# Performance work log

Measured on AMD Instinct MI355X. Metric: run time of the kernel, lower is better.

The kernel has to match this reference:

```python
import jax, jax.numpy as jnp
import numpy as np

S, B, C, H = 8192, 4, 512, 8
D = C // H
EPS = 1e-6


def setup_inputs() -> dict:
    key = jax.random.key(0)
    ks = jax.random.split(key, 11)
    scale = 1.0 / np.sqrt(C)
    return {
        "query": jax.random.normal(ks[0], (S, B, C), jnp.float32),
        "key": jax.random.normal(ks[1], (S, B, C), jnp.float32),
        "value": jax.random.normal(ks[2], (S, B, C), jnp.float32),
        "Wq": jax.random.normal(ks[3], (C, C), jnp.float32) * scale,
        "bq": jnp.zeros((C,), jnp.float32),
        "Wk": jax.random.normal(ks[4], (C, C), jnp.float32) * scale,
        "bk": jnp.zeros((C,), jnp.float32),
        "Wv": jax.random.normal(ks[5], (C, C), jnp.float32) * scale,
        "bv": jnp.zeros((C,), jnp.float32),
        "Wp": jax.random.normal(ks[6], (C, C), jnp.float32) * scale,
        "bp": jnp.zeros((C,), jnp.float32),
    }


def _elu_fm(x):
    # ELU(x) + 1 feature map
    return jax.nn.elu(x) + 1.0


def _heads(x, W, b):
    # x: [B, N, C] -> [B, H, N, D]
    y = x @ W.T + b
    Bb, N, _ = y.shape
    return y.reshape(Bb, N, H, D).transpose(0, 2, 1, 3)


def reference(query, key, value, Wq, bq, Wk, bk, Wv, bv, Wp, bp):
    # inputs [S, B, C] -> batch-first [B, S, C]
    q_in = query.transpose(1, 0, 2)
    k_in = key.transpose(1, 0, 2)
    v_in = value.transpose(1, 0, 2)

    q = _elu_fm(_heads(q_in, Wq, bq))   # [B,H,N,D]
    k = _elu_fm(_heads(k_in, Wk, bk))   # [B,H,N,D]
    v = _heads(v_in, Wv, bv)            # [B,H,N,D]

    # linear attention: O(N) kv-sum formulation
    kv = jnp.einsum('bhnd,bhnf->bhdf', k, v)       # [B,H,D,D]
    k_sum = k.sum(axis=2)                          # [B,H,D]
    qkv = jnp.einsum('bhnd,bhdf->bhnf', q, kv)     # [B,H,N,D]
    denom = jnp.einsum('bhnd,bhd->bhn', q, k_sum)  # [B,H,N]
    y = qkv / (denom[..., None] + EPS)

    # merge heads, output projection, back to [S, B, C]
    y = y.transpose(0, 2, 1, 3).reshape(q_in.shape[0], q_in.shape[1], C)
    out = y @ Wp.T + bp
    return out.transpose(1, 0, 2)
```

## Files before the change

kernel.cpp:

```cpp
#include <hip/hip_runtime.h>
#include <hip/hip_bf16.h>
#include <math.h>

#define S_LEN 8192
#define BATCH 4
#define CDIM  512
#define HEADS 8
#define DDIM  64
#define MROWS (S_LEN * BATCH)
#define EPS_F 1e-6f

typedef __attribute__((ext_vector_type(8))) short     short8_t;
typedef __attribute__((ext_vector_type(4))) float     f32x4;
typedef unsigned short ushort_t;
typedef __attribute__((ext_vector_type(8))) unsigned short ushort8_t;

static __device__ __forceinline__ ushort_t f2bf(float f) {
  __hip_bfloat16 h = __float2bfloat16(f);
  return *(ushort_t*)&h;
}

static __device__ __forceinline__ void gl2lds16(const ushort_t* g, ushort_t* l) {
  __builtin_amdgcn_global_load_lds((const __attribute__((address_space(1))) void*)g,
                                   (__attribute__((address_space(3))) void*)l,
                                   16, 0, 0);
}

__global__ __launch_bounds__(256)
void cvtW_pack(const float* __restrict__ a, const float* __restrict__ b,
               const float* __restrict__ c, const float* __restrict__ d,
               ushort_t* __restrict__ oa, ushort_t* __restrict__ ob,
               ushort_t* __restrict__ oc, ushort_t* __restrict__ od) {
  const float* src = (blockIdx.y == 0) ? a : (blockIdx.y == 1) ? b :
                     (blockIdx.y == 2) ? c : d;
  ushort_t* dst    = (blockIdx.y == 0) ? oa : (blockIdx.y == 1) ? ob :
                     (blockIdx.y == 2) ? oc : od;
  const size_t i = ((size_t)blockIdx.x * 256 + threadIdx.x) * 8;
  const int n  = (int)(i >> 9);
  const int k0 = (int)(i & 511);
  const float4 x = *(const float4*)&src[i];
  const float4 y = *(const float4*)&src[i + 4];
  ushort8_t p;
  p[0] = f2bf(x.x); p[1] = f2bf(x.y); p[2] = f2bf(x.z); p[3] = f2bf(x.w);
  p[4] = f2bf(y.x); p[5] = f2bf(y.y); p[6] = f2bf(y.z); p[7] = f2bf(y.w);
  const int kf   = k0 >> 5;
  const int lane = ((k0 >> 3) & 3) * 16 + (n & 15);
  const int nfg  = n >> 4;
  *(ushort8_t*)&dst[(((size_t)nfg * 16 + kf) * 64 + lane) * 8] = p;
}

template<int AF32, int OUTF32>
static __device__ __forceinline__
void gemm256_body(const void* __restrict__ Av, const ushort_t* __restrict__ Wpk,
                  const float* __restrict__ bias, void* __restrict__ Yv,
                  const bool act, const int m0, const int n0, ushort_t* lds) {
  const int t    = threadIdx.x;
  const int w    = t >> 6;
  const int lane = t & 63;
  const int lr   = lane & 15;
  const int lk8  = (lane >> 4) * 8;
  const int wm   = (w >> 2) * 128;
  const int wn   = (w & 3) * 64;

  const float*    Xf = (const float*)Av;
  const ushort_t* Ah = (const ushort_t*)Av;

  ushort_t* A0 = lds;
  ushort_t* A1 = lds + 16384;
  ushort_t* B0 = lds + 32768;
  ushort_t* B1 = lds + 49152;

  f32x4 ar[4][2];

  auto regloadA = [&](int kt) {
    #pragma unroll
    for (int j = 0; j < 4; ++j) {
      const int fid = w * 4 + j;
      const size_t g = (size_t)(m0 + (fid >> 1) * 16 + lr) * CDIM +
                       kt + (fid & 1) * 32 + lk8;
      ar[j][0] = __builtin_nontemporal_load((const f32x4*)&Xf[g]);
      ar[j][1] = __builtin_nontemporal_load((const f32x4*)&Xf[g + 4]);
    }
  };
  auto stageA_f32 = [&](ushort_t* Ab) {
    #pragma unroll
    for (int j = 0; j < 4; ++j) {
      const int fid = w * 4 + j;
      short8_t v;
      v[0] = (short)f2bf(ar[j][0][0]); v[1] = (short)f2bf(ar[j][0][1]);
      v[2] = (short)f2bf(ar[j][0][2]); v[3] = (short)f2bf(ar[j][0][3]);
      v[4] = (short)f2bf(ar[j][1][0]); v[5] = (short)f2bf(ar[j][1][1]);
      v[6] = (short)f2bf(ar[j][1][2]); v[7] = (short)f2bf(ar[j][1][3]);
      *(short8_t*)&lds[(Ab - lds) + (size_t)fid * 512 + lane * 8] = v;
    }
  };
  auto stageA_bf16 = [&](ushort_t* Ab, int kt) {
    #pragma unroll
    for (int j = 0; j < 4; ++j) {
      const int fid = w * 4 + j;
      const ushort_t* g = Ah + (size_t)(m0 + (fid >> 1) * 16 + lr) * CDIM +
                          kt + (fid & 1) * 32 + lk8;
      gl2lds16(g, &Ab[fid * 512]);
    }
  };
  auto stageB = [&](ushort_t* Bb, int kt) {
    #pragma unroll
    for (int j = 0; j < 4; ++j) {
      const int fid = w * 4 + j;
      const size_t idx = ((size_t)((n0 >> 4) + (fid >> 1)) * 16 +
                          (kt >> 5) + (fid & 1));
      gl2lds16(Wpk + idx * 512 + lane * 8, &Bb[fid * 512]);
    }
  };

  f32x4 acc[8][4];
  #pragma unroll
  for (int mf = 0; mf < 8; ++mf)
    #pragma unroll
    for (int nf = 0; nf < 4; ++nf)
      acc[mf][nf] = (f32x4){0.f, 0.f, 0.f, 0.f};

  auto compute = [&](const ushort_t* Ab, const ushort_t* Bb) {
    short8_t bfr[2][4];
    #pragma unroll
    for (int kf = 0; kf < 2; ++kf)
      #pragma unroll
      for (int nf = 0; nf < 4; ++nf) {
        const int fidb = ((wn >> 4) + nf) * 2 + kf;
        bfr[kf][nf] = *(const short8_t*)&Bb[fidb * 512 + lane * 8];
      }
    #pragma unroll
    for (int mf = 0; mf < 8; ++mf) {
      const int fa = ((wm >> 4) + mf) * 2;
      const short8_t a0 = *(const short8_t*)&Ab[(fa + 0) * 512 + lane * 8];
      const short8_t a1 = *(const short8_t*)&Ab[(fa + 1) * 512 + lane * 8];
      #pragma unroll
      for (int nf = 0; nf < 4; ++nf)
        acc[mf][nf] = __builtin_amdgcn_mfma_f32_16x16x32_bf16(
            a0, bfr[0][nf], acc[mf][nf], 0, 0, 0);
      #pragma unroll
      for (int nf = 0; nf < 4; ++nf)
        acc[mf][nf] = __builtin_amdgcn_mfma_f32_16x16x32_bf16(
            a1, bfr[1][nf], acc[mf][nf], 0, 0, 0);
    }
  };

  if (AF32) {
    regloadA(0);
    stageA_f32(A0);
    stageB(B0, 0);
    regloadA(64);
  } else {
    stageA_bf16(A0, 0);
    stageB(B0, 0);
  }
  __syncthreads();

  #pragma unroll
  for (int ks = 0; ks < 8; ++ks) {
    ushort_t* curA = (ks & 1) ? A1 : A0;
    ushort_t* curB = (ks & 1) ? B1 : B0;
    ushort_t* nxtA = (ks & 1) ? A0 : A1;
    ushort_t* nxtB = (ks & 1) ? B0 : B1;
    if (ks < 7) {
      if (AF32) {
        stageA_f32(nxtA);
        if (ks + 2 < 8) regloadA((ks + 2) * 64);
      } else {
        stageA_bf16(nxtA, (ks + 1) * 64);
      }
      stageB(nxtB, (ks + 1) * 64);
    }
    compute(curA, curB);
    __syncthreads();
  }

  if (OUTF32) {
    float* Yf = (float*)Yv;
    #pragma unroll
    for (int nf = 0; nf < 4; ++nf) {
      const int col = n0 + wn + nf * 16 + lr;
      const float bi = bias[col];
      #pragma unroll
      for (int mf = 0; mf < 8; ++mf) {
        #pragma unroll
        for (int r = 0; r < 4; ++r) {
          const int m = m0 + wm + mf * 16 + (lane >> 4) * 4 + r;
          __builtin_nontemporal_store(acc[mf][nf][r] + bi,
                                      &Yf[(size_t)m * CDIM + col]);
        }
      }
    }
  } else {
    ushort_t* Yh = (ushort_t*)Yv;
    #pragma unroll
    for (int nf = 0; nf < 4; ++nf) {
      const int col = wn + nf * 16 + lr;
      const float bi = bias[n0 + col];
      #pragma unroll
      for (int mf = 0; mf < 8; ++mf) {
        #pragma unroll
        for (int r = 0; r < 4; ++r) {
          const int row = wm + mf * 16 + (lane >> 4) * 4 + r;
          float vv = acc[mf][nf][r] + bi;
          if (act) vv = (vv > 0.f) ? (vv + 1.f) : expf(vv);
          lds[row * 256 + col] = f2bf(vv);
        }
      }
    }
    __syncthreads();
    #pragma unroll
    for (int it = 0; it < 16; ++it) {
      const int u   = it * 512 + t;
      const int row = u >> 5;
      const int c8  = (u & 31) * 8;
      const short8_t v = *(const short8_t*)&lds[u * 8];
      __builtin_nontemporal_store(
          v, (short8_t*)&Yh[(size_t)(m0 + row) * CDIM + n0 + c8]);
    }
  }
}

__global__ __launch_bounds__(512)
void proj3_256(const float* __restrict__ Xq, const float* __restrict__ Xk,
               const float* __restrict__ Xv,
               const ushort_t* __restrict__ Wqp, const ushort_t* __restrict__ Wkp,
               const ushort_t* __restrict__ Wvp,
               const float* __restrict__ bq, const float* __restrict__ bk,
               const float* __restrict__ bv,
               ushort_t* __restrict__ Yq, ushort_t* __restrict__ Yk,
               ushort_t* __restrict__ Yv) {
  extern __shared__ ushort_t lds[];
  const int z = blockIdx.z;
  const float*    X    = (z == 0) ? Xq : (z == 1) ? Xk : Xv;
  const ushort_t* Wpk  = (z == 0) ? Wqp : (z == 1) ? Wkp : Wvp;
  const float*    bias = (z == 0) ? bq : (z == 1) ? bk : bv;
  ushort_t*       Y    = (z == 0) ? Yq : (z == 1) ? Yk : Yv;
  gemm256_body<1, 0>(X, Wpk, bias, Y, z < 2,
                     blockIdx.y * 256, blockIdx.x * 256, lds);
}

__global__ __launch_bounds__(512)
void outp_256(const ushort_t* __restrict__ A, const ushort_t* __restrict__ Wpk,
              const float* __restrict__ bias, float* __restrict__ Y) {
  extern __shared__ ushort_t lds[];
  gemm256_body<0, 1>(A, Wpk, bias, Y, false,
                     blockIdx.y * 256, blockIdx.x * 256, lds);
}

__global__ __launch_bounds__(256)
void gemm_kv(const ushort_t* __restrict__ Kb, const ushort_t* __restrict__ Vb,
             float* __restrict__ kvpart, float* __restrict__ ksumpart) {
  __shared__ __align__(16) ushort_t klds[8192];
  __shared__ __align__(16) ushort_t vlds[8192];
  const int bh    = blockIdx.x;
  const int chunk = blockIdx.y;
  const int b = bh >> 3, h = bh & 7;
  const int t = threadIdx.x;
  const int w = t >> 6;
  const int lane = t & 63;

  f32x4 acc[4];
  #pragma unroll
  for (int fg = 0; fg < 4; ++fg) acc[fg] = (f32x4){0.f, 0.f, 0.f, 0.f};
  f32x4 accs = (f32x4){0.f, 0.f, 0.f, 0.f};

  short8_t ones;
  #pragma unroll
  for (int i = 0; i < 8; ++i) ones[i] = (short)0x3F80;

  for (int round = 0; round < 4; ++round) {
    const int sbase = chunk * 512 + round * 128;
    __syncthreads();
    #pragma unroll
    for (int i = 0; i < 4; ++i) {
      const int idx  = i * 256 + t;
      const int sl   = idx >> 3;
      const int d8   = idx & 7;
      const size_t src = (size_t)((sbase + sl) * BATCH + b) * CDIM + h * DDIM + d8 * 8;
      const ushort8_t kp = *(const ushort8_t*)&Kb[src];
      const ushort8_t vp = *(const ushort8_t*)&Vb[src];
      const int sb  = sl >> 5;
      const int j   = sl & 7;
      const int lp0 = (d8 & 1) * 8 + ((sl >> 3) & 3) * 16;
      const int dg  = d8 >> 1;
      const int kbase = ((sb * 4 + dg) * 64 + lp0) * 8 + j;
      #pragma unroll
      for (int e = 0; e < 8; ++e) {
        klds[kbase + e * 8] = kp[e];
        vlds[kbase + e * 8] = vp[e];
      }
    }
    __syncthreads();
    #pragma unroll
    for (int sb = 0; sb < 4; ++sb) {
      const short8_t af = *(const short8_t*)&klds[((sb * 4 + w) * 64 + lane) * 8];
      accs = __builtin_amdgcn_mfma_f32_16x16x32_bf16(af, ones, accs, 0, 0, 0);
      #pragma unroll
      for (int fg = 0; fg < 4; ++fg) {
        const short8_t bf = *(const short8_t*)&vlds[((sb * 4 + fg) * 64 + lane) * 8];
        acc[fg] = __builtin_amdgcn_mfma_f32_16x16x32_bf16(af, bf, acc[fg], 0, 0, 0);
      }
    }
  }

  const size_t obase = ((size_t)bh * 16 + chunk) * 64;
  #pragma unroll
  for (int fg = 0; fg < 4; ++fg)
    #pragma unroll
    for (int r = 0; r < 4; ++r) {
      const int d = w * 16 + (lane >> 4) * 4 + r;
      kvpart[(obase + d) * 64 + fg * 16 + (lane & 15)] = acc[fg][r];
    }
  if ((lane & 15) == 0) {
    #pragma unroll
    for (int r = 0; r < 4; ++r)
      ksumpart[obase + w * 16 + (lane >> 4) * 4 + r] = accs[r];
  }
}

__global__ __launch_bounds__(256)
void kv_finish(const float* __restrict__ kvpart, const float* __restrict__ ksumpart,
               ushort_t* __restrict__ kvT) {
  const int bh = blockIdx.x;
  const int t  = threadIdx.x;
  for (int idx = t; idx < 4096; idx += 256) {
    const int d = idx >> 6, f = idx & 63;
    float s = 0.f;
    for (int c = 0; c < 16; ++c)
      s += kvpart[(((size_t)bh * 16 + c) * 64 + d) * 64 + f];
    kvT[((size_t)bh * 80 + f) * 64 + d] = f2bf(s);
  }
  if (t < 64) {
    float s = 0.f;
    for (int c = 0; c < 16; ++c)
      s += ksumpart[((size_t)bh * 16 + c) * 64 + t];
    kvT[((size_t)bh * 80 + 64) * 64 + t] = f2bf(s);
  }
  for (int i = t; i < 15 * 64; i += 256)
    kvT[((size_t)bh * 80 + 65) * 64 + i] = 0;
}

__global__ __launch_bounds__(256)
void gemm_qkv(ushort_t* __restrict__ Qb, const ushort_t* __restrict__ kvT) {
  __shared__ __align__(16) ushort_t alds[8192];
  __shared__ __align__(16) ushort_t blds[5120];
  const int bh    = blockIdx.x;
  const int chunk = blockIdx.y;
  const int b = bh >> 3, h = bh & 7;
  const int t = threadIdx.x;
  const int w = t >> 6;
  const int lane = t & 63;
  const int lr = lane & 15;
  const int lk = (lane >> 4) * 8;

  #pragma unroll
  for (int i = 0; i < 4; ++i) {
    const int fidx = w * 4 + i;
    const int ks = fidx >> 3, fm = fidx & 7;
    const ushort_t* src = Qb +
        (size_t)((chunk * 128 + fm * 16 + lr) * BATCH + b) * CDIM +
        h * DDIM + ks * 32 + lk;
    gl2lds16(src, &alds[fidx * 512]);
  }
  for (int idx = w; idx < 10; idx += 4) {
    const int ks = idx / 5, fg = idx % 5;
    const ushort_t* src = kvT + (size_t)(bh * 80 + fg * 16 + lr) * 64 + ks * 32 + lk;
    gl2lds16(src, &blds[idx * 512]);
  }
  __syncthreads();

  f32x4 acc[2][5];
  #pragma unroll
  for (int mi = 0; mi < 2; ++mi)
    #pragma unroll
    for (int fg = 0; fg < 5; ++fg)
      acc[mi][fg] = (f32x4){0.f, 0.f, 0.f, 0.f};

  #pragma unroll
  for (int ks = 0; ks < 2; ++ks) {
    short8_t af[2], bf[5];
    #pragma unroll
    for (int mi = 0; mi < 2; ++mi)
      af[mi] = *(const short8_t*)&alds[(ks * 8 + w * 2 + mi) * 512 + lane * 8];
    #pragma unroll
    for (int fg = 0; fg < 5; ++fg)
      bf[fg] = *(const short8_t*)&blds[(ks * 5 + fg) * 512 + lane * 8];
    #pragma unroll
    for (int mi = 0; mi < 2; ++mi)
      #pragma unroll
      for (int fg = 0; fg < 5; ++fg)
        acc[mi][fg] = __builtin_amdgcn_mfma_f32_16x16x32_bf16(
            af[mi], bf[fg], acc[mi][fg], 0, 0, 0);
  }

  #pragma unroll
  for (int mi = 0; mi < 2; ++mi) {
    #pragma unroll
    for (int r = 0; r < 4; ++r) {
      const float dv  = __shfl(acc[mi][4][r], lane & 48);
      const float inv = 1.f / (dv + EPS_F);
      const int s = chunk * 128 + w * 32 + mi * 16 + (lane >> 4) * 4 + r;
      const size_t rowb = (size_t)(s * BATCH + b) * CDIM + h * DDIM;
      #pragma unroll
      for (int fg = 0; fg < 4; ++fg)
        Qb[rowb + fg * 16 + lr] = f2bf(acc[mi][fg][r] * inv);
    }
  }
}

extern "C" void kernel_launch(void* const* d_in, const int* in_sizes, int n_in,
                              void* d_out, int out_size, void* d_ws, size_t ws_size,
                              hipStream_t stream) {
  const float* q_in = (const float*)d_in[0];
  const float* k_in = (const float*)d_in[1];
  const float* v_in = (const float*)d_in[2];
  const float* Wq   = (const float*)d_in[3];
  const float* bq   = (const float*)d_in[4];
  const float* Wk   = (const float*)d_in[5];
  const float* bk   = (const float*)d_in[6];
  const float* Wv   = (const float*)d_in[7];
  const float* bv   = (const float*)d_in[8];
  const float* Wp   = (const float*)d_in[9];
  const float* bp   = (const float*)d_in[10];
  float* out = (float*)d_out;

  const size_t NTOK = (size_t)MROWS * CDIM;
  const size_t NW   = (size_t)CDIM * CDIM;
  ushort_t* Wqp    = (ushort_t*)d_ws;
  ushort_t* Wkp    = Wqp + NW;
  ushort_t* Wvp    = Wkp + NW;
  ushort_t* Wpp    = Wvp + NW;
  ushort_t* qbuf   = Wpp + NW;
  ushort_t* kbuf   = qbuf + NTOK;
  ushort_t* vbuf   = kbuf + NTOK;
  ushort_t* kvT    = vbuf + NTOK;
  float* kvpart    = (float*)(kvT + (size_t)32 * 80 * 64);
  float* ksumpart  = kvpart + (size_t)512 * 64 * 64;

  const dim3 blk(256);
  const size_t LDSB = 131072;

  cvtW_pack<<<dim3(128, 4), blk, 0, stream>>>(Wq, Wk, Wv, Wp,
                                              Wqp, Wkp, Wvp, Wpp);

  proj3_256<<<dim3(CDIM / 256, MROWS / 256, 3), dim3(512), LDSB, stream>>>(
      q_in, k_in, v_in, Wqp, Wkp, Wvp, bq, bk, bv, qbuf, kbuf, vbuf);

  gemm_kv<<<dim3(32, 16), blk, 0, stream>>>(kbuf, vbuf, kvpart, ksumpart);
  kv_finish<<<dim3(32), blk, 0, stream>>>(kvpart, ksumpart, kvT);

  gemm_qkv<<<dim3(32, 64), blk, 0, stream>>>(qbuf, kvT);

  outp_256<<<dim3(CDIM / 256, MROWS / 256), dim3(512), LDSB, stream>>>(
      qbuf, Wpp, bp, out);
}
```

Baseline: 241.5 us.

## Replace syncthreads with partial vmcnt waits and raise MFMA priority in GEMM

```diff
diff --git a/kernel.cpp b/kernel.cpp
--- a/kernel.cpp
+++ b/kernel.cpp
@@ -25,6 +25,11 @@
                                    (__attribute__((address_space(3))) void*)l,
                                    16, 0, 0);
 }
+
+#define WAIT_VM12 asm volatile("s_waitcnt vmcnt(12) lgkmcnt(0)" ::: "memory")
+#define WAIT_VM8  asm volatile("s_waitcnt vmcnt(8) lgkmcnt(0)"  ::: "memory")
+#define WAIT_VM4  asm volatile("s_waitcnt vmcnt(4) lgkmcnt(0)"  ::: "memory")
+#define WAIT_VM0  asm volatile("s_waitcnt vmcnt(0) lgkmcnt(0)"  ::: "memory")
 
 __global__ __launch_bounds__(256)
 void cvtW_pack(const float* __restrict__ a, const float* __restrict__ b,
@@ -91,7 +96,7 @@
       v[2] = (short)f2bf(ar[j][0][2]); v[3] = (short)f2bf(ar[j][0][3]);
       v[4] = (short)f2bf(ar[j][1][0]); v[5] = (short)f2bf(ar[j][1][1]);
       v[6] = (short)f2bf(ar[j][1][2]); v[7] = (short)f2bf(ar[j][1][3]);
-      *(short8_t*)&lds[(Ab - lds) + (size_t)fid * 512 + lane * 8] = v;
+      *(short8_t*)&Ab[(size_t)fid * 512 + lane * 8] = v;
     }
   };
   auto stageA_bf16 = [&](ushort_t* Ab, int kt) {
@@ -129,6 +134,7 @@
         const int fidb = ((wn >> 4) + nf) * 2 + kf;
         bfr[kf][nf] = *(const short8_t*)&Bb[fidb * 512 + lane * 8];
       }
+    __builtin_amdgcn_s_setprio(1);
     #pragma unroll
     for (int mf = 0; mf < 8; ++mf) {
       const int fa = ((wm >> 4) + mf) * 2;
@@ -143,6 +149,7 @@
         acc[mf][nf] = __builtin_amdgcn_mfma_f32_16x16x32_bf16(
             a1, bfr[1][nf], acc[mf][nf], 0, 0, 0);
     }
+    __builtin_amdgcn_s_setprio(0);
   };
 
   if (AF32) {
@@ -154,26 +161,39 @@
     stageA_bf16(A0, 0);
     stageB(B0, 0);
   }
-  __syncthreads();
-
-  #pragma unroll
-  for (int ks = 0; ks < 8; ++ks) {
-    ushort_t* curA = (ks & 1) ? A1 : A0;
-    ushort_t* curB = (ks & 1) ? B1 : B0;
-    ushort_t* nxtA = (ks & 1) ? A0 : A1;
-    ushort_t* nxtB = (ks & 1) ? B0 : B1;
-    if (ks < 7) {
-      if (AF32) {
-        stageA_f32(nxtA);
-        if (ks + 2 < 8) regloadA((ks + 2) * 64);
-      } else {
-        stageA_bf16(nxtA, (ks + 1) * 64);
-      }
-      stageB(nxtB, (ks + 1) * 64);
-    }
-    compute(curA, curB);
-    __syncthreads();
-  }
+
+#define KSTEP(ks, WAITM)                                                   \
+  do {                                                                     \
+    ushort_t* curA = ((ks) & 1) ? A1 : A0;                                 \
+    ushort_t* curB = ((ks) & 1) ? B1 : B0;                                 \
+    ushort_t* nxtA = ((ks) & 1) ? A0 : A1;                                 \
+    ushort_t* nxtB = ((ks) & 1) ? B0 : B1;                                 \
+    if ((ks) < 7) {                                                        \
+      if (AF32) {                                                          \
+        stageA_f32(nxtA);                                                  \
+        if ((ks) + 2 < 8) regloadA(((ks) + 2) * 64);                       \
+      } else {                                                             \
+        stageA_bf16(nxtA, ((ks) + 1) * 64);                                \
+      }                                                                    \
+      stageB(nxtB, ((ks) + 1) * 64);                                       \
+    }                                                                      \
+    WAITM;                                                                 \
+    __builtin_amdgcn_s_barrier();                                          \
+    __builtin_amdgcn_sched_barrier(0);                                     \
+    compute(curA, curB);                                                   \
+    __builtin_amdgcn_s_barrier();                                          \
+  } while (0)
+
+  if (AF32) {
+    KSTEP(0, WAIT_VM12); KSTEP(1, WAIT_VM12); KSTEP(2, WAIT_VM12);
+    KSTEP(3, WAIT_VM12); KSTEP(4, WAIT_VM12); KSTEP(5, WAIT_VM12);
+    KSTEP(6, WAIT_VM4);  KSTEP(7, WAIT_VM0);
+  } else {
+    KSTEP(0, WAIT_VM8); KSTEP(1, WAIT_VM8); KSTEP(2, WAIT_VM8);
+    KSTEP(3, WAIT_VM8); KSTEP(4, WAIT_VM8); KSTEP(5, WAIT_VM8);
+    KSTEP(6, WAIT_VM8); KSTEP(7, WAIT_VM0);
+  }
+#undef KSTEP
 
   if (OUTF32) {
     float* Yf = (float*)Yv;
```

Measured after the change: 241.4 us. About the same (-0.0%).
